# Kernel tuning notes

Measured on AMD Instinct MI355X. Metric: run time of the kernel, lower is better.

The kernel has to match this reference:

```python
import jax, jax.numpy as jnp
import numpy as np

B, N, H, HEADS = 8, 1024, 512, 4  # batch graphs, nodes/graph, graph_hsz, attention heads
R = 64  # relations per graph (passthrough)


def setup_inputs() -> dict:
    key = jax.random.key(0)
    k1, k2, k3, k4, k5, k6, k7 = jax.random.split(key, 7)
    adjs = jax.random.randint(k1, (B, N, N), 0, 2, dtype=jnp.int32)  # 0 => masked
    nodes = jax.random.normal(k2, (B, N, H), dtype=jnp.float32)
    triples = jax.random.normal(k3, (B, R, H), dtype=jnp.float32)   # unused in gat path
    relations = jax.random.normal(k4, (B, R, H), dtype=jnp.float32)  # passthrough
    node_num = jnp.full((B,), N, dtype=jnp.int32)  # all graphs full => no padding branch
    s = 1.0 / np.sqrt(H)
    Wq = (jax.random.normal(k5, (H, H), dtype=jnp.float32) * s)
    Wk = (jax.random.normal(k6, (H, H), dtype=jnp.float32) * s)
    Wv = (jax.random.normal(k7, (H, H), dtype=jnp.float32) * s)
    return {"adjs": adjs, "triples": triples, "nodes": nodes, "node_num": node_num,
            "relations": relations, "Wq": Wq, "Wk": Wk, "Wv": Wv}


def reference(adjs, triples, nodes, node_num, relations, Wq, Wk, Wv):
    b, n, h = nodes.shape
    dk = h // HEADS
    scale = 1.0 / jnp.sqrt(jnp.float32(h))  # torch divides by sqrt(key_dim)=sqrt(H)

    def to_heads(x, W):  # [B,N,H] -> [B,heads,N,dk]; matches split(dim=-1)+stack
        return (x @ W).reshape(b, n, HEADS, dk).transpose(0, 2, 1, 3)

    Q = to_heads(nodes, Wq)
    K = to_heads(nodes, Wk)
    V = to_heads(nodes, Wv)
    att = jnp.einsum('bhnd,bhmd->bhnm', Q, K) * scale
    att = jnp.where((adjs == 0)[:, None, :, :], -jnp.inf, att)
    p = jax.nn.softmax(att, axis=-1)  # dropout_p = blockdrop = 0.0 => identity
    out = jnp.einsum('bhnm,bhmd->bhnd', p, V)
    out = out.transpose(0, 2, 1, 3).reshape(b, n, h)  # concat heads along feature dim
    out = jax.nn.relu(out)
    return (out, relations)
```

## Files before the change

### kernel.cpp

```cpp
#include <hip/hip_runtime.h>
#include <stdint.h>

typedef __attribute__((ext_vector_type(4))) float f32x4;
typedef __attribute__((ext_vector_type(8))) short bf16x8;
typedef unsigned long long ull;

#define GLB_AS const __attribute__((address_space(1)))
#define LDS_AS __attribute__((address_space(3)))

__device__ __forceinline__ short f2bf(float f) {
    union { float f; unsigned u; } x; x.f = f;
    unsigned r = x.u + 0x7FFFu + ((x.u >> 16) & 1u);
    return (short)(r >> 16);
}

__global__ void k_pre(const float* __restrict__ nodes, short* __restrict__ nodes_bf,
                      const float* __restrict__ Wq, const float* __restrict__ Wk,
                      const float* __restrict__ Wv, short* __restrict__ WT,
                      const int* __restrict__ adjs, unsigned* __restrict__ packed) {
    int bi = blockIdx.x, tid = threadIdx.x;
    if (bi < 2048) {
        int i = (bi * 256 + tid) * 8;
        float4 a = *(const float4*)(nodes + i);
        float4 b = *(const float4*)(nodes + i + 4);
        bf16x8 v;
        v[0] = f2bf(a.x); v[1] = f2bf(a.y); v[2] = f2bf(a.z); v[3] = f2bf(a.w);
        v[4] = f2bf(b.x); v[5] = f2bf(b.y); v[6] = f2bf(b.z); v[7] = f2bf(b.w);
        *(bf16x8*)(nodes_bf + i) = v;
    } else if (bi < 5120) {
        int g = (bi - 2048) * 256 + tid;
        int j = g >> 9, k = g & 511;
        int w = j >> 9, n = j & 511;
        const float* W = (w == 0) ? Wq : (w == 1) ? Wk : Wv;
        WT[g] = f2bf(W[k * 512 + n]);
    } else {
        int g = (bi - 5120) * 256 + tid;
        int wv = g >> 6, lane = g & 63;
        ull m = __ballot(adjs[(size_t)wv * 64 + lane] != 0);
        if (lane == 0) *(ull*)(packed + (size_t)wv * 2) = m;
    }
}

__global__ __launch_bounds__(256) void k_gemm_qkv(const short* __restrict__ A,
                                                  const short* __restrict__ WT,
                                                  short* __restrict__ C) {
    __shared__ short Asm[2][128 * 32];
    __shared__ short Bsm[2][128 * 32];
    const int tid = threadIdx.x;
    const int l = tid & 63, w = tid >> 6;
    const int wr = w >> 1, wc = w & 1;
    const int c16 = l & 15, g = l >> 4;
    const int wg = blockIdx.x;
    const int swz = (wg & 7) * 96 + (wg >> 3);
    const int row0 = (swz / 12) * 128, n0 = (swz % 12) * 128;
    f32x4 acc[4][4] = {};

    auto stage = [&](int kt, int bsel) {
        const int k0 = kt * 32;
#pragma unroll
        for (int i = 0; i < 2; ++i) {
            int ch = tid + 256 * i;
            int r = ch >> 2, gc = ch & 3;
            __builtin_amdgcn_global_load_lds((GLB_AS unsigned*)(A + (row0 + r) * 512 + k0 + 8 * gc),
                                             (LDS_AS unsigned*)(&Asm[bsel][ch * 8]), 16, 0, 0);
            __builtin_amdgcn_global_load_lds((GLB_AS unsigned*)(WT + (n0 + r) * 512 + k0 + 8 * gc),
                                             (LDS_AS unsigned*)(&Bsm[bsel][ch * 8]), 16, 0, 0);
        }
    };

    stage(0, 0);
    asm volatile("s_waitcnt vmcnt(0)" ::: "memory");
    __syncthreads();

    for (int kt = 0; kt < 16; ++kt) {
        const int cur = kt & 1;
        if (kt < 15) stage(kt + 1, cur ^ 1);
        bf16x8 af[4], bfr[4];
#pragma unroll
        for (int mf = 0; mf < 4; ++mf)
            af[mf] = *(const bf16x8*)&Asm[cur][(wr * 64 + mf * 16 + c16) * 32 + 8 * g];
#pragma unroll
        for (int nf = 0; nf < 4; ++nf)
            bfr[nf] = *(const bf16x8*)&Bsm[cur][(wc * 64 + nf * 16 + c16) * 32 + 8 * g];
#pragma unroll
        for (int mf = 0; mf < 4; ++mf)
#pragma unroll
            for (int nf = 0; nf < 4; ++nf)
                acc[mf][nf] = __builtin_amdgcn_mfma_f32_16x16x32_bf16(af[mf], bfr[nf], acc[mf][nf], 0, 0, 0);
        asm volatile("s_waitcnt vmcnt(0)" ::: "memory");
        __syncthreads();
    }
#pragma unroll
    for (int mf = 0; mf < 4; ++mf)
#pragma unroll
        for (int nf = 0; nf < 4; ++nf)
#pragma unroll
            for (int r = 0; r < 4; ++r) {
                int row = row0 + wr * 64 + mf * 16 + 4 * g + r;
                int col = n0 + wc * 64 + nf * 16 + c16;
                C[row * 1536 + col] = f2bf(acc[mf][nf][r]);
            }
}

__global__ __launch_bounds__(256) void k_mid(const short* __restrict__ QKV, short* __restrict__ Vt,
                                             const float* __restrict__ rel_in, float* __restrict__ rel_out) {
    __shared__ short tile[64 * 65];
    const int bi = blockIdx.x, t = threadIdx.x;
    if (bi >= 1024) {
        int i = ((bi - 1024) * 256 + t) * 4;
        *(float4*)(rel_out + i) = *(const float4*)(rel_in + i);
        return;
    }
    const int b = bi >> 7, n0 = ((bi >> 3) & 15) * 64, d0 = (bi & 7) * 64;
#pragma unroll
    for (int i = 0; i < 16; ++i) {
        int idx = t + 256 * i;
        int nn = idx >> 6, dd = idx & 63;
        tile[nn * 65 + dd] = QKV[(b * 1024 + n0 + nn) * 1536 + 1024 + d0 + dd];
    }
    __syncthreads();
#pragma unroll
    for (int i = 0; i < 16; ++i) {
        int idx = t + 256 * i;
        int dd = idx >> 6, nn = idx & 63;
        Vt[(b * 512 + d0 + dd) * 1024 + n0 + nn] = tile[nn * 65 + dd];
    }
}

__global__ __launch_bounds__(256) void k_attn(const short* __restrict__ QKV, const short* __restrict__ Vt,
                                              const unsigned* __restrict__ packed, float* __restrict__ out) {
    __shared__ short Ksm[2][64 * 128];
    __shared__ short Vsm[2][128 * 64];
    __shared__ short Psm[4][16 * 68];
    const int bh = blockIdx.x;
    const int b = bh >> 2, h = bh & 3;
    const int q0 = blockIdx.y * 64;
    const int tid = threadIdx.x, l = tid & 63, wid = tid >> 6;
    const int c16 = l & 15, g = l >> 4;
    const int qw = q0 + wid * 16;
    const float kscale = 0.06375872022286384f;

    bf16x8 aq[4];
    const short* Qrow = QKV + (size_t)(b * 1024 + qw + c16) * 1536 + h * 128;
#pragma unroll
    for (int kf = 0; kf < 4; ++kf)
        aq[kf] = *(const bf16x8*)(Qrow + kf * 32 + 8 * g);

    f32x4 acc_o[8] = {};
    float l_lane = 0.f;

    const short* Kbase = QKV + (size_t)(b * 1024) * 1536 + 512 + h * 128;
    const short* Vtbase = Vt + (size_t)(b * 512 + h * 128) * 1024;
    const ull* adjq = (const ull*)packed + (size_t)(b * 1024 + qw + c16) * 16;

    auto stage = [&](int t, int bsel) {
        const int m0 = t * 64;
#pragma unroll
        for (int i = 0; i < 4; ++i) {
            int ch = tid + 256 * i;
            int mr = ch >> 4, gc = ch & 15;
            int gs = gc ^ (mr & 7);
            __builtin_amdgcn_global_load_lds((GLB_AS unsigned*)(Kbase + (size_t)(m0 + mr) * 1536 + 8 * gs),
                                             (LDS_AS unsigned*)(&Ksm[bsel][ch * 8]), 16, 0, 0);
        }
#pragma unroll
        for (int i = 0; i < 4; ++i) {
            int ch = tid + 256 * i;
            int dr = ch >> 3, gc = ch & 7;
            int gs = gc ^ (dr & 7);
            __builtin_amdgcn_global_load_lds((GLB_AS unsigned*)(Vtbase + (size_t)dr * 1024 + m0 + 8 * gs),
                                             (LDS_AS unsigned*)(&Vsm[bsel][ch * 8]), 16, 0, 0);
        }
    };

    ull mcur, mnxt = 0;
    mcur = adjq[0];
    stage(0, 0);
    asm volatile("s_waitcnt vmcnt(0)" ::: "memory");
    __builtin_amdgcn_s_barrier();

    for (int t = 0; t < 16; ++t) {
        const int cur = t & 1;
        if (t < 15) {
            mnxt = adjq[t + 1];
            stage(t + 1, cur ^ 1);
        }

        f32x4 s[4] = {};
        __builtin_amdgcn_s_setprio(1);
#pragma unroll
        for (int nf = 0; nf < 4; ++nf) {
            const int mrow = nf * 16 + c16;
#pragma unroll
            for (int kf = 0; kf < 4; ++kf) {
                int chunk = (kf * 4 + g) ^ (mrow & 7);
                bf16x8 ak = *(const bf16x8*)&Ksm[cur][mrow * 128 + chunk * 8];
                s[nf] = __builtin_amdgcn_mfma_f32_16x16x32_bf16(ak, aq[kf], s[nf], 0, 0, 0);
            }
        }
        __builtin_amdgcn_s_setprio(0);

        unsigned mlo = (unsigned)mcur, mhi = (unsigned)(mcur >> 32);
#pragma unroll
        for (int nf = 0; nf < 4; ++nf) {
            unsigned hw = (nf < 2) ? mlo : mhi;
            unsigned nib = (hw >> ((nf & 1) * 16 + 4 * g)) & 15u;
            float p0 = (nib & 1u) ? __builtin_amdgcn_exp2f(s[nf][0] * kscale) : 0.f;
            float p1 = (nib & 2u) ? __builtin_amdgcn_exp2f(s[nf][1] * kscale) : 0.f;
            float p2 = (nib & 4u) ? __builtin_amdgcn_exp2f(s[nf][2] * kscale) : 0.f;
            float p3 = (nib & 8u) ? __builtin_amdgcn_exp2f(s[nf][3] * kscale) : 0.f;
            l_lane += (p0 + p1) + (p2 + p3);
            unsigned lo, hi;
            asm("v_cvt_pk_bf16_f32 %0, %1, %2" : "=v"(lo) : "v"(p0), "v"(p1));
            asm("v_cvt_pk_bf16_f32 %0, %1, %2" : "=v"(hi) : "v"(p2), "v"(p3));
            ull wv = ((ull)hi << 32) | lo;
            *(ull*)&Psm[wid][c16 * 68 + nf * 16 + 4 * g] = wv;
        }

        if (t < 15) { asm volatile("s_waitcnt vmcnt(9)" ::: "memory"); }
        else        { asm volatile("s_waitcnt vmcnt(0)" ::: "memory"); }
        __builtin_amdgcn_s_barrier();

        __builtin_amdgcn_s_setprio(1);
#pragma unroll
        for (int ks = 0; ks < 2; ++ks) {
            union { ull u[2]; bf16x8 v; } ap;
            ap.u[0] = *(const ull*)&Psm[wid][c16 * 68 + ks * 32 + 8 * g];
            ap.u[1] = *(const ull*)&Psm[wid][c16 * 68 + ks * 32 + 8 * g + 4];
#pragma unroll
            for (int df = 0; df < 8; ++df) {
                const int drow = df * 16 + c16;
                int chunk = (ks * 4 + g) ^ (drow & 7);
                bf16x8 bv = *(const bf16x8*)&Vsm[cur][drow * 64 + chunk * 8];
                acc_o[df] = __builtin_amdgcn_mfma_f32_16x16x32_bf16(ap.v, bv, acc_o[df], 0, 0, 0);
            }
        }
        __builtin_amdgcn_s_setprio(0);

        mcur = mnxt;

        if (t < 15) {
            asm volatile("s_waitcnt vmcnt(4)" ::: "memory");
            __builtin_amdgcn_s_barrier();
        }
    }

    l_lane += __shfl_xor(l_lane, 16);
    l_lane += __shfl_xor(l_lane, 32);
    float inv_l[4];
#pragma unroll
    for (int r = 0; r < 4; ++r)
        inv_l[r] = 1.f / __shfl(l_lane, 4 * g + r);

#pragma unroll
    for (int df = 0; df < 8; ++df)
#pragma unroll
        for (int r = 0; r < 4; ++r) {
            int q = qw + 4 * g + r;
            float o = fmaxf(acc_o[df][r] * inv_l[r], 0.f);
            out[(size_t)(b * 1024 + q) * 512 + h * 128 + df * 16 + c16] = o;
        }
}

extern "C" void kernel_launch(void* const* d_in, const int* in_sizes, int n_in,
                              void* d_out, int out_size, void* d_ws, size_t ws_size,
                              hipStream_t stream) {
    const int*   adjs      = (const int*)d_in[0];
    const float* nodes     = (const float*)d_in[2];
    const float* relations = (const float*)d_in[4];
    const float* Wq        = (const float*)d_in[5];
    const float* Wk        = (const float*)d_in[6];
    const float* Wv        = (const float*)d_in[7];

    char* ws = (char*)d_ws;
    short* nodes_bf   = (short*)(ws);
    short* WT         = (short*)(ws + 8388608);
    short* QKV        = (short*)(ws + 9961472);
    short* Vt         = (short*)(ws + 35127296);
    unsigned* adjpack = (unsigned*)(ws + 43515904);

    float* out     = (float*)d_out;
    float* out_rel = out + 4194304;

    k_pre<<<dim3(37888), dim3(256), 0, stream>>>(nodes, nodes_bf, Wq, Wk, Wv, WT, adjs, adjpack);
    k_gemm_qkv<<<dim3(768), dim3(256), 0, stream>>>(nodes_bf, WT, QKV);
    k_mid<<<dim3(1280), dim3(256), 0, stream>>>(QKV, Vt, relations, out_rel);
    k_attn<<<dim3(32, 16), dim3(256), 0, stream>>>(QKV, Vt, adjpack, out);
}
```

Measured before the change: 81.21 us.

## Switch attention to 32x32 MFMA with register-resident P and folded scale

Rewrites the attention kernel to use 32x32x16 bf16 MFMA tiles, with 32 queries per wave and 128 per block. This halves the grid and doubles K/V reuse per LDS stage. The P matrix is rearranged into the A-operand layout with cross-half lane shuffles instead of being round-tripped through LDS. The softmax scale is folded into the Q columns in the QKV GEMM epilogue, which removes the per-element multiply. In exchange, register pressure rises (launch_bounds 256,2) and fewer blocks are launched, so there is less parallelism per CU.

After: 86.64 us. +6.7%, slower.

```diff
diff --git a/kernel.cpp b/kernel.cpp
--- a/kernel.cpp
+++ b/kernel.cpp
@@ -2,6 +2,7 @@
 #include <stdint.h>
 
 typedef __attribute__((ext_vector_type(4))) float f32x4;
+typedef __attribute__((ext_vector_type(16))) float f32x16;
 typedef __attribute__((ext_vector_type(8))) short bf16x8;
 typedef unsigned long long ull;
 
@@ -93,13 +94,15 @@
 #pragma unroll
     for (int mf = 0; mf < 4; ++mf)
 #pragma unroll
-        for (int nf = 0; nf < 4; ++nf)
+        for (int nf = 0; nf < 4; ++nf) {
+            const float cs = (n0 + wc * 64 + nf * 16 < 512) ? 0.06375872022286384f : 1.0f;
 #pragma unroll
             for (int r = 0; r < 4; ++r) {
                 int row = row0 + wr * 64 + mf * 16 + 4 * g + r;
                 int col = n0 + wc * 64 + nf * 16 + c16;
-                C[row * 1536 + col] = f2bf(acc[mf][nf][r]);
-            }
+                C[row * 1536 + col] = f2bf(acc[mf][nf][r] * cs);
+            }
+        }
 }
 
 __global__ __launch_bounds__(256) void k_mid(const short* __restrict__ QKV, short* __restrict__ Vt,
@@ -127,31 +130,29 @@
     }
 }
 
-__global__ __launch_bounds__(256) void k_attn(const short* __restrict__ QKV, const short* __restrict__ Vt,
-                                              const unsigned* __restrict__ packed, float* __restrict__ out) {
+__global__ __launch_bounds__(256, 2) void k_attn(const short* __restrict__ QKV, const short* __restrict__ Vt,
+                                                 const unsigned* __restrict__ packed, float* __restrict__ out) {
     __shared__ short Ksm[2][64 * 128];
     __shared__ short Vsm[2][128 * 64];
-    __shared__ short Psm[4][16 * 68];
     const int bh = blockIdx.x;
     const int b = bh >> 2, h = bh & 3;
-    const int q0 = blockIdx.y * 64;
+    const int q0 = blockIdx.y * 128;
     const int tid = threadIdx.x, l = tid & 63, wid = tid >> 6;
-    const int c16 = l & 15, g = l >> 4;
-    const int qw = q0 + wid * 16;
-    const float kscale = 0.06375872022286384f;
-
-    bf16x8 aq[4];
-    const short* Qrow = QKV + (size_t)(b * 1024 + qw + c16) * 1536 + h * 128;
-#pragma unroll
-    for (int kf = 0; kf < 4; ++kf)
-        aq[kf] = *(const bf16x8*)(Qrow + kf * 32 + 8 * g);
-
-    f32x4 acc_o[8] = {};
+    const int l31 = l & 31, hi = l >> 5;
+    const int qw = q0 + wid * 32;
+
+    bf16x8 aq[8];
+    const short* Qb = QKV + (size_t)(b * 1024 + qw + l31) * 1536 + h * 128;
+#pragma unroll
+    for (int kk = 0; kk < 8; ++kk)
+        aq[kk] = *(const bf16x8*)(Qb + kk * 16 + hi * 8);
+
+    f32x16 acc[4] = {};
     float l_lane = 0.f;
 
     const short* Kbase = QKV + (size_t)(b * 1024) * 1536 + 512 + h * 128;
     const short* Vtbase = Vt + (size_t)(b * 512 + h * 128) * 1024;
-    const ull* adjq = (const ull*)packed + (size_t)(b * 1024 + qw + c16) * 16;
+    const ull* adjq = (const ull*)packed + (size_t)(b * 1024 + qw + l31) * 16;
 
     auto stage = [&](int t, int bsel) {
         const int m0 = t * 64;
@@ -173,8 +174,7 @@
         }
     };
 
-    ull mcur, mnxt = 0;
-    mcur = adjq[0];
+    ull mcur = adjq[0], mnxt = 0;
     stage(0, 0);
     asm volatile("s_waitcnt vmcnt(0)" ::: "memory");
     __builtin_amdgcn_s_barrier();
@@ -186,36 +186,56 @@
             stage(t + 1, cur ^ 1);
         }
 
-        f32x4 s[4] = {};
+        f32x16 s[2] = {};
         __builtin_amdgcn_s_setprio(1);
 #pragma unroll
-        for (int nf = 0; nf < 4; ++nf) {
-            const int mrow = nf * 16 + c16;
-#pragma unroll
-            for (int kf = 0; kf < 4; ++kf) {
-                int chunk = (kf * 4 + g) ^ (mrow & 7);
-                bf16x8 ak = *(const bf16x8*)&Ksm[cur][mrow * 128 + chunk * 8];
-                s[nf] = __builtin_amdgcn_mfma_f32_16x16x32_bf16(ak, aq[kf], s[nf], 0, 0, 0);
-            }
-        }
+        for (int kk = 0; kk < 8; ++kk)
+#pragma unroll
+            for (int mm = 0; mm < 2; ++mm) {
+                const int row = mm * 32 + l31;
+                const int chunk = (2 * kk + hi) ^ (row & 7);
+                bf16x8 ak = *(const bf16x8*)&Ksm[cur][row * 128 + chunk * 8];
+                s[mm] = __builtin_amdgcn_mfma_f32_32x32x16_bf16(ak, aq[kk], s[mm], 0, 0, 0);
+            }
         __builtin_amdgcn_s_setprio(0);
 
-        unsigned mlo = (unsigned)mcur, mhi = (unsigned)(mcur >> 32);
-#pragma unroll
-        for (int nf = 0; nf < 4; ++nf) {
-            unsigned hw = (nf < 2) ? mlo : mhi;
-            unsigned nib = (hw >> ((nf & 1) * 16 + 4 * g)) & 15u;
-            float p0 = (nib & 1u) ? __builtin_amdgcn_exp2f(s[nf][0] * kscale) : 0.f;
-            float p1 = (nib & 2u) ? __builtin_amdgcn_exp2f(s[nf][1] * kscale) : 0.f;
-            float p2 = (nib & 4u) ? __builtin_amdgcn_exp2f(s[nf][2] * kscale) : 0.f;
-            float p3 = (nib & 8u) ? __builtin_amdgcn_exp2f(s[nf][3] * kscale) : 0.f;
-            l_lane += (p0 + p1) + (p2 + p3);
-            unsigned lo, hi;
-            asm("v_cvt_pk_bf16_f32 %0, %1, %2" : "=v"(lo) : "v"(p0), "v"(p1));
-            asm("v_cvt_pk_bf16_f32 %0, %1, %2" : "=v"(hi) : "v"(p2), "v"(p3));
-            ull wv = ((ull)hi << 32) | lo;
-            *(ull*)&Psm[wid][c16 * 68 + nf * 16 + 4 * g] = wv;
-        }
+        unsigned pk[2][4][2];
+#pragma unroll
+        for (int mm = 0; mm < 2; ++mm) {
+            const unsigned mshift = (unsigned)(mcur >> (32 * mm + 4 * hi));
+#pragma unroll
+            for (int j = 0; j < 4; ++j) {
+                float p[4];
+#pragma unroll
+                for (int r = 0; r < 4; ++r) {
+                    float e = __builtin_amdgcn_exp2f(s[mm][4 * j + r]);
+                    p[r] = ((mshift >> (8 * j + r)) & 1u) ? e : 0.f;
+                    l_lane += p[r];
+                }
+                asm("v_cvt_pk_bf16_f32 %0, %1, %2" : "=v"(pk[mm][j][0]) : "v"(p[0]), "v"(p[1]));
+                asm("v_cvt_pk_bf16_f32 %0, %1, %2" : "=v"(pk[mm][j][1]) : "v"(p[2]), "v"(p[3]));
+            }
+        }
+
+        union fragu { unsigned u[4]; bf16x8 v; };
+        fragu frag[4];
+#pragma unroll
+        for (int mm = 0; mm < 2; ++mm)
+#pragma unroll
+            for (int kh = 0; kh < 2; ++kh) {
+                unsigned a0 = pk[mm][2 * kh][0], a1 = pk[mm][2 * kh][1];
+                unsigned b0 = pk[mm][2 * kh + 1][0], b1 = pk[mm][2 * kh + 1][1];
+                unsigned rx0 = (unsigned)__shfl_xor((int)a0, 32);
+                unsigned rx1 = (unsigned)__shfl_xor((int)a1, 32);
+                unsigned rx2 = (unsigned)__shfl_xor((int)b0, 32);
+                unsigned rx3 = (unsigned)__shfl_xor((int)b1, 32);
+                fragu f;
+                f.u[0] = hi ? rx2 : a0;
+                f.u[1] = hi ? rx3 : a1;
+                f.u[2] = hi ? b0 : rx0;
+                f.u[3] = hi ? b1 : rx1;
+                frag[2 * mm + kh] = f;
+            }
 
         if (t < 15) { asm volatile("s_waitcnt vmcnt(9)" ::: "memory"); }
         else        { asm volatile("s_waitcnt vmcnt(0)" ::: "memory"); }
@@ -223,18 +243,14 @@
 
         __builtin_amdgcn_s_setprio(1);
 #pragma unroll
-        for (int ks = 0; ks < 2; ++ks) {
-            union { ull u[2]; bf16x8 v; } ap;
-            ap.u[0] = *(const ull*)&Psm[wid][c16 * 68 + ks * 32 + 8 * g];
-            ap.u[1] = *(const ull*)&Psm[wid][c16 * 68 + ks * 32 + 8 * g + 4];
-#pragma unroll
-            for (int df = 0; df < 8; ++df) {
-                const int drow = df * 16 + c16;
-                int chunk = (ks * 4 + g) ^ (drow & 7);
-                bf16x8 bv = *(const bf16x8*)&Vsm[cur][drow * 64 + chunk * 8];
-                acc_o[df] = __builtin_amdgcn_mfma_f32_16x16x32_bf16(ap.v, bv, acc_o[df], 0, 0, 0);
-            }
-        }
+        for (int ks = 0; ks < 4; ++ks)
+#pragma unroll
+            for (int dd = 0; dd < 4; ++dd) {
+                const int row = dd * 32 + l31;
+                const int chunk = (2 * ks + hi) ^ (row & 7);
+                bf16x8 bv = *(const bf16x8*)&Vsm[cur][row * 64 + chunk * 8];
+                acc[dd] = __builtin_amdgcn_mfma_f32_32x32x16_bf16(frag[ks].v, bv, acc[dd], 0, 0, 0);
+            }
         __builtin_amdgcn_s_setprio(0);
 
         mcur = mnxt;
@@ -245,21 +261,25 @@
         }
     }
 
-    l_lane += __shfl_xor(l_lane, 16);
     l_lane += __shfl_xor(l_lane, 32);
-    float inv_l[4];
-#pragma unroll
-    for (int r = 0; r < 4; ++r)
-        inv_l[r] = 1.f / __shfl(l_lane, 4 * g + r);
-
-#pragma unroll
-    for (int df = 0; df < 8; ++df)
-#pragma unroll
-        for (int r = 0; r < 4; ++r) {
-            int q = qw + 4 * g + r;
-            float o = fmaxf(acc_o[df][r] * inv_l[r], 0.f);
-            out[(size_t)(b * 1024 + q) * 512 + h * 128 + df * 16 + c16] = o;
-        }
+    float inv_own = 1.f / l_lane;
+    float iv[16];
+#pragma unroll
+    for (int j = 0; j < 4; ++j)
+#pragma unroll
+        for (int r = 0; r < 4; ++r)
+            iv[4 * j + r] = __shfl(inv_own, r + 8 * j + 4 * hi);
+
+#pragma unroll
+    for (int dd = 0; dd < 4; ++dd)
+#pragma unroll
+        for (int j = 0; j < 4; ++j)
+#pragma unroll
+            for (int r = 0; r < 4; ++r) {
+                int q32 = r + 8 * j + 4 * hi;
+                float o = fmaxf(acc[dd][4 * j + r] * iv[4 * j + r], 0.f);
+                out[(size_t)(b * 1024 + qw + q32) * 512 + h * 128 + dd * 32 + l31] = o;
+            }
 }
 
 extern "C" void kernel_launch(void* const* d_in, const int* in_sizes, int n_in,
@@ -285,5 +305,5 @@
     k_pre<<<dim3(37888), dim3(256), 0, stream>>>(nodes, nodes_bf, Wq, Wk, Wv, WT, adjs, adjpack);
     k_gemm_qkv<<<dim3(768), dim3(256), 0, stream>>>(nodes_bf, WT, QKV);
     k_mid<<<dim3(1280), dim3(256), 0, stream>>>(QKV, Vt, relations, out_rel);
-    k_attn<<<dim3(32, 16), dim3(256), 0, stream>>>(QKV, Vt, adjpack, out);
-}
+    k_attn<<<dim3(32, 8), dim3(256), 0, stream>>>(QKV, Vt, adjpack, out);
+}
```
